# Kernel tuning notes

Hardware: AMD Instinct MI355X
Metric: run time of the kernel (lower is better)

Reference implementation:

```python
import jax, jax.numpy as jnp
import numpy as np

B, IN, OUT, G = 8192, 512, 512, 20


def setup_inputs() -> dict:
    key = jax.random.key(0)
    k1, k2, k3 = jax.random.split(key, 3)
    x = jax.random.normal(k1, (B, IN), dtype=jnp.float32)
    coeffs = jax.random.normal(k2, (OUT, IN, G + 1), dtype=jnp.float32) * 0.1
    base_w = jax.random.normal(k3, (OUT, IN), dtype=jnp.float32) * 0.1
    return {"x": x, "coeffs": coeffs, "base_w": base_w}


def reference(x, coeffs, base_w):
    g = coeffs.shape[-1] - 1  # grid_size
    xc = jnp.clip(x, -1.0, 1.0)
    base = jax.nn.silu(xc) @ base_w.T  # [B, out]
    x_grid = (xc + 1.0) * 0.5 * g  # [B, in], in [0, g]
    idx = jnp.clip(jnp.floor(x_grid).astype(jnp.int32), 0, g - 1)  # [B, in]
    t = x_grid - idx.astype(x.dtype)  # [B, in]
    b, n = x.shape
    bi = jnp.arange(b)[:, None]
    fi = jnp.arange(n)[None, :]
    # Sparse interpolation weights over grid bins: 2 nonzeros per (b, i).
    w = jnp.zeros((b, n, g + 1), dtype=x.dtype)
    w = w.at[bi, fi, idx].add(1.0 - t)
    w = w.at[bi, fi, idx + 1].add(t)  # idx+1 <= g since idx <= g-1
    # y[b,o] = sum_i sum_g w[b,i,g] * coeffs[o,i,g]
    y = jnp.einsum('big,oig->bo', w, coeffs)
    return base + y
```

## Files before the change

### kernel.cpp

```cpp
#include <hip/hip_runtime.h>
#include <stdint.h>


typedef short v8s __attribute__((ext_vector_type(8)));
typedef float v4f __attribute__((ext_vector_type(4)));

#define B_DIM 8192
#define IN_DIM 512
#define OUT_DIM 512
#define G_DIM 20
#define FPT 4
#define KT_TOTAL (IN_DIM / FPT)
#define KSPLIT 3
#define BM 128
#define BN 128
#define CHUNKS 12
#define PLANE 2048
#define TILE_BYTES (CHUNKS * PLANE)

#define P_BYTES ((size_t)IN_DIM * B_DIM * 8)
#define WT_BYTES ((size_t)(OUT_DIM / BN) * KT_TOTAL * TILE_BYTES)
#define PART_ELEMS ((size_t)B_DIM * OUT_DIM)
#define WS_NEED (P_BYTES + WT_BYTES + (size_t)KSPLIT * PART_ELEMS * 2)

#define PACK_BLKS ((B_DIM / 64) * (IN_DIM / 64))
#define WPACK_BLKS ((OUT_DIM * IN_DIM) / 256)

static __device__ __forceinline__ unsigned f2bf(float f) {
  unsigned u = __builtin_bit_cast(unsigned, f);
  return (u + 0x7fffu + ((u >> 16) & 1u)) >> 16;
}

static __device__ __forceinline__ float bflo(unsigned u) {
  return __builtin_bit_cast(float, u << 16);
}
static __device__ __forceinline__ float bfhi(unsigned u) {
  return __builtin_bit_cast(float, u & 0xffff0000u);
}

__global__ void zero_out_kernel(uint4* __restrict__ out) {
  out[(size_t)blockIdx.x * 256 + threadIdx.x] = uint4{0u, 0u, 0u, 0u};
}

__global__ void pack_fused_kernel(const float* __restrict__ x, uint2* __restrict__ P,
                                  const float* __restrict__ coeffs,
                                  const float* __restrict__ base_w,
                                  char* __restrict__ Wt) {
  __shared__ uint2 tile[64 * 65];
  const int t = threadIdx.x;
  if (blockIdx.x < PACK_BLKS) {
    const int b0 = (blockIdx.x & (B_DIM / 64 - 1)) * 64;
    const int i0 = (blockIdx.x / (B_DIM / 64)) * 64;
    const int tr = t >> 6;
    const int tc = t & 63;
#pragma unroll
    for (int it = 0; it < 16; ++it) {
      int br = it * 4 + tr;
      float xv = x[(size_t)(b0 + br) * IN_DIM + i0 + tc];
      float xc = fminf(fmaxf(xv, -1.0f), 1.0f);
      float xg = (xc + 1.0f) * 10.0f;
      int idx = (int)floorf(xg);
      idx = idx < 0 ? 0 : (idx > G_DIM - 1 ? G_DIM - 1 : idx);
      float tt = xg - (float)idx;
      float sl = xc / (1.0f + __expf(-xc));
      uint2 pv;
      pv.x = f2bf(1.0f - tt) | (f2bf(tt) << 16);
      pv.y = (unsigned)idx | (f2bf(sl) << 16);
      tile[tc * 65 + br] = pv;
    }
    __syncthreads();
#pragma unroll
    for (int it = 0; it < 16; ++it) {
      int ir = it * 4 + tr;
      P[(size_t)(i0 + ir) * B_DIM + b0 + tc] = tile[ir * 65 + tc];
    }
  } else {
    const unsigned u = (blockIdx.x - PACK_BLKS) * 256 + t;
    const int s = u >> 9;
    const int w = u & 511;
    const int row = w >> 2;
    const int f = w & 3;
    const int n_blk = s / KT_TOTAL;
    const int kt = s - n_blk * KT_TOTAL;
    const int o = n_blk * 128 + row;
    const int i = kt * 4 + f;
    const size_t g = (size_t)o * IN_DIM + i;
    const float* c = coeffs + g * 21;
    float cf[21];
#pragma unroll
    for (int j = 0; j < 21; ++j) cf[j] = c[j];
    float bw = base_w[g];
    unsigned d[12];
#pragma unroll
    for (int j = 0; j < 10; ++j) d[j] = f2bf(cf[2 * j]) | (f2bf(cf[2 * j + 1]) << 16);
    d[10] = f2bf(cf[20]) | (f2bf(bw) << 16);
    d[11] = 0u;
    char* slab = Wt + (size_t)s * TILE_BYTES;
#pragma unroll
    for (int p = 0; p < 3; ++p)
      *(uint4*)(slab + (3 * f + p) * PLANE + row * 16) =
          uint4{d[4 * p], d[4 * p + 1], d[4 * p + 2], d[4 * p + 3]};
  }
}

__global__ void reduce_kernel(const uint4* __restrict__ p, v4f* __restrict__ out) {
  size_t i = (size_t)blockIdx.x * 256 + threadIdx.x;
  const size_t q = PART_ELEMS / 8;
  uint4 a = p[i], b = p[i + q], c = p[i + 2 * q];
  v4f lo, hi;
  lo[0] = bflo(a.x) + bflo(b.x) + bflo(c.x);
  hi[0] = bfhi(a.x) + bfhi(b.x) + bfhi(c.x);
  lo[1] = bflo(a.y) + bflo(b.y) + bflo(c.y);
  hi[1] = bfhi(a.y) + bfhi(b.y) + bfhi(c.y);
  lo[2] = bflo(a.z) + bflo(b.z) + bflo(c.z);
  hi[2] = bfhi(a.z) + bfhi(b.z) + bfhi(c.z);
  lo[3] = bflo(a.w) + bflo(b.w) + bflo(c.w);
  hi[3] = bfhi(a.w) + bfhi(b.w) + bfhi(c.w);
  v4f o0 = {lo[0], hi[0], lo[1], hi[1]};
  v4f o1 = {lo[2], hi[2], lo[3], hi[3]};
  out[2 * i] = o0;
  out[2 * i + 1] = o1;
}

static __device__ __forceinline__ void stage_strip(char* abase, uint2 pv) {
  const uint4 zz = {0u, 0u, 0u, 0u};
#pragma unroll
  for (int p = 0; p < 3; ++p) *(uint4*)(abase + p * PLANE) = zz;
  const int idx = (int)(pv.y & 0xffffu);
  const int s1 = idx + 1;
  *(unsigned short*)(abase + ((idx >> 3) << 11) + ((idx & 7) << 1)) =
      (unsigned short)pv.x;
  *(unsigned short*)(abase + ((s1 >> 3) << 11) + ((s1 & 7) << 1)) =
      (unsigned short)(pv.x >> 16);
  *(unsigned short*)(abase + 2 * PLANE + 10) = (unsigned short)(pv.y >> 16);
}

template <bool ATOMIC>
__global__ __launch_bounds__(256, 3) void kan_gemm(const uint2* __restrict__ P,
                                                   const char* __restrict__ Wt,
                                                   unsigned short* __restrict__ part,
                                                   float* __restrict__ outA) {
  __shared__ uint4 lds4[TILE_BYTES / 16];
  char* Ab = (char*)lds4;
  const int t = threadIdx.x;
  const int lane = t & 63;
  const int wv = t >> 6;
  const int wm = wv >> 1, wn = wv & 1;
  const int b0 = blockIdx.x * BM;
  const int n_blk = blockIdx.y;
  const int z = blockIdx.z;
  const int kt0 = (z * KT_TOTAL) / KSPLIT;
  const int ktend = ((z + 1) * KT_TOTAL) / KSPLIT;

  v4f acc[4][4];
  const v4f z4 = {0.f, 0.f, 0.f, 0.f};
#pragma unroll
  for (int ii = 0; ii < 4; ++ii)
#pragma unroll
    for (int jj = 0; jj < 4; ++jj) acc[ii][jj] = z4;

  char* abase0 = Ab + 3 * wv * PLANE + lane * 16;
  char* abase1 = Ab + 3 * wv * PLANE + (lane + 64) * 16;
  uint2 pv0 = P[(size_t)(kt0 * 4 + wv) * B_DIM + b0 + lane];
  uint2 pv1 = P[(size_t)(kt0 * 4 + wv) * B_DIM + b0 + lane + 64];

  const int r16 = lane & 15;
  const int q16 = lane >> 4;

  const uint4* wbase = (const uint4*)(Wt + (size_t)n_blk * KT_TOTAL * TILE_BYTES);
  int bidx[3][4];
#pragma unroll
  for (int s = 0; s < 3; ++s)
#pragma unroll
    for (int cn = 0; cn < 4; ++cn)
      bidx[s][cn] = (s * 4 + q16) * 128 + wn * 64 + cn * 16 + r16;

  for (int kt = kt0; kt < ktend; ++kt) {
    __syncthreads();

    const uint4* wsrc = wbase + (size_t)kt * (TILE_BYTES / 16);
    uint4 bv[3][4];
#pragma unroll
    for (int s = 0; s < 3; ++s)
#pragma unroll
      for (int cn = 0; cn < 4; ++cn)
        bv[s][cn] = wsrc[bidx[s][cn]];

    const int ktn = (kt + 1 < ktend) ? kt + 1 : kt;
    uint2 pn0 = P[(size_t)(ktn * 4 + wv) * B_DIM + b0 + lane];
    uint2 pn1 = P[(size_t)(ktn * 4 + wv) * B_DIM + b0 + lane + 64];

    stage_strip(abase0, pv0);
    stage_strip(abase1, pv1);
    pv0 = pn0;
    pv1 = pn1;

    __syncthreads();

#pragma unroll
    for (int s = 0; s < 3; ++s) {
      const int chunk = s * 4 + q16;
      v8s af[4];
#pragma unroll
      for (int rm = 0; rm < 4; ++rm) {
        int row = wm * 64 + rm * 16 + r16;
        af[rm] = *(const v8s*)(Ab + chunk * PLANE + row * 16);
      }
#pragma unroll
      for (int rm = 0; rm < 4; ++rm)
#pragma unroll
        for (int cn = 0; cn < 4; ++cn)
          acc[rm][cn] = __builtin_amdgcn_mfma_f32_16x16x32_bf16(
              af[rm], __builtin_bit_cast(v8s, bv[s][cn]), acc[rm][cn], 0, 0, 0);
    }
  }

  const int q4 = (lane >> 4) * 4;
  if (ATOMIC) {
#pragma unroll
    for (int rm = 0; rm < 4; ++rm)
#pragma unroll
      for (int cn = 0; cn < 4; ++cn)
#pragma unroll
        for (int r = 0; r < 4; ++r) {
          int row = b0 + wm * 64 + rm * 16 + q4 + r;
          int col = n_blk * BN + wn * 64 + cn * 16 + r16;
          atomicAdd(outA + (size_t)row * OUT_DIM + col, acc[rm][cn][r]);
        }
  } else {
    unsigned short* mypart = part + (size_t)z * PART_ELEMS;
#pragma unroll
    for (int rm = 0; rm < 4; ++rm)
#pragma unroll
      for (int cn = 0; cn < 4; ++cn)
#pragma unroll
        for (int r = 0; r < 4; ++r) {
          int row = b0 + wm * 64 + rm * 16 + q4 + r;
          int col = n_blk * BN + wn * 64 + cn * 16 + r16;
          mypart[(size_t)row * OUT_DIM + col] = (unsigned short)f2bf(acc[rm][cn][r]);
        }
  }
}

extern "C" void kernel_launch(void* const* d_in, const int* in_sizes, int n_in,
                              void* d_out, int out_size, void* d_ws, size_t ws_size,
                              hipStream_t stream) {
  const float* x = (const float*)d_in[0];
  const float* coeffs = (const float*)d_in[1];
  const float* base_w = (const float*)d_in[2];
  float* out = (float*)d_out;

  uint2* P = (uint2*)d_ws;
  char* Wt = (char*)d_ws + P_BYTES;
  unsigned short* part = (unsigned short*)((char*)d_ws + P_BYTES + WT_BYTES);

  pack_fused_kernel<<<PACK_BLKS + WPACK_BLKS, 256, 0, stream>>>(x, P, coeffs, base_w, Wt);

  if (ws_size >= WS_NEED) {
    kan_gemm<false><<<dim3(B_DIM / BM, OUT_DIM / BN, KSPLIT), 256, 0, stream>>>(P, Wt, part, out);
    reduce_kernel<<<(int)(PART_ELEMS / 8 / 256), 256, 0, stream>>>((const uint4*)part, (v4f*)out);
  } else {
    zero_out_kernel<<<(int)((PART_ELEMS * 4) / 4096), 256, 0, stream>>>((uint4*)out);
    kan_gemm<true><<<dim3(B_DIM / BM, OUT_DIM / BN, KSPLIT), 256, 0, stream>>>(P, Wt, part, out);
  }
}
```

Measured before the change: 180.5 us.

## Double-buffer LDS A-tile and prefetch weights to remove per-iteration barrier

The shared A-tile becomes two buffers, so staging for step k+1 overlaps the MFMA work of step k. This leaves one __syncthreads per iteration instead of two. Weight fragments for the next k-step are loaded into registers after the current MFMAs, giving them a full iteration to arrive. Instead of zeroing three 16-byte planes per strip each step, each thread now clears only the two slots it wrote previously in that buffer. The cost is double the LDS use (48KB per block with 3 blocks per CU requested), plus extra live registers for the prefetched weights and cursor pointers.

```diff
diff --git a/kernel.cpp b/kernel.cpp
--- a/kernel.cpp
+++ b/kernel.cpp
@@ -122,17 +122,22 @@
   out[2 * i + 1] = o1;
 }
 
-static __device__ __forceinline__ void stage_strip(char* abase, uint2 pv) {
-  const uint4 zz = {0u, 0u, 0u, 0u};
-#pragma unroll
-  for (int p = 0; p < 3; ++p) *(uint4*)(abase + p * PLANE) = zz;
+static __device__ __forceinline__ int slot_off(int slot) {
+  return ((slot >> 3) << 11) + ((slot & 7) << 1);
+}
+
+static __device__ __forceinline__ void stage_inc(char* abase, uint2 pv,
+                                                 char*& ca, char*& cb) {
+  *(unsigned short*)ca = 0;
+  *(unsigned short*)cb = 0;
   const int idx = (int)(pv.y & 0xffffu);
-  const int s1 = idx + 1;
-  *(unsigned short*)(abase + ((idx >> 3) << 11) + ((idx & 7) << 1)) =
-      (unsigned short)pv.x;
-  *(unsigned short*)(abase + ((s1 >> 3) << 11) + ((s1 & 7) << 1)) =
-      (unsigned short)(pv.x >> 16);
+  char* wa = abase + slot_off(idx);
+  char* wb = abase + slot_off(idx + 1);
+  *(unsigned short*)wa = (unsigned short)pv.x;
+  *(unsigned short*)wb = (unsigned short)(pv.x >> 16);
   *(unsigned short*)(abase + 2 * PLANE + 10) = (unsigned short)(pv.y >> 16);
+  ca = wa;
+  cb = wb;
 }
 
 template <bool ATOMIC>
@@ -140,8 +145,7 @@
                                                    const char* __restrict__ Wt,
                                                    unsigned short* __restrict__ part,
                                                    float* __restrict__ outA) {
-  __shared__ uint4 lds4[TILE_BYTES / 16];
-  char* Ab = (char*)lds4;
+  __shared__ uint4 lds4[2 * TILE_BYTES / 16];
   const int t = threadIdx.x;
   const int lane = t & 63;
   const int wv = t >> 6;
@@ -159,10 +163,35 @@
 #pragma unroll
     for (int jj = 0; jj < 4; ++jj) acc[ii][jj] = z4;
 
-  char* abase0 = Ab + 3 * wv * PLANE + lane * 16;
-  char* abase1 = Ab + 3 * wv * PLANE + (lane + 64) * 16;
-  uint2 pv0 = P[(size_t)(kt0 * 4 + wv) * B_DIM + b0 + lane];
-  uint2 pv1 = P[(size_t)(kt0 * 4 + wv) * B_DIM + b0 + lane + 64];
+  {
+    const uint4 zz = {0u, 0u, 0u, 0u};
+#pragma unroll
+    for (int j = 0; j < 12; ++j) lds4[t + 256 * j] = zz;
+  }
+  __syncthreads();
+
+  char* ab0[2];
+  char* ab1[2];
+#pragma unroll
+  for (int p = 0; p < 2; ++p) {
+    ab0[p] = (char*)lds4 + p * TILE_BYTES + 3 * wv * PLANE + lane * 16;
+    ab1[p] = (char*)lds4 + p * TILE_BYTES + 3 * wv * PLANE + (lane + 64) * 16;
+  }
+  char* c0a[2] = {ab0[0], ab0[1]};
+  char* c0b[2] = {ab0[0] + 2, ab0[1] + 2};
+  char* c1a[2] = {ab1[0], ab1[1]};
+  char* c1b[2] = {ab1[0] + 2, ab1[1] + 2};
+
+  {
+    const int p0 = kt0 & 1;
+    uint2 s0 = P[(size_t)(kt0 * 4 + wv) * B_DIM + b0 + lane];
+    uint2 s1 = P[(size_t)(kt0 * 4 + wv) * B_DIM + b0 + lane + 64];
+    stage_inc(ab0[p0], s0, c0a[p0], c0b[p0]);
+    stage_inc(ab1[p0], s1, c1a[p0], c1b[p0]);
+  }
+  const int ktp = (kt0 + 1 < ktend) ? kt0 + 1 : ktend - 1;
+  uint2 pv0 = P[(size_t)(ktp * 4 + wv) * B_DIM + b0 + lane];
+  uint2 pv1 = P[(size_t)(ktp * 4 + wv) * B_DIM + b0 + lane + 64];
 
   const int r16 = lane & 15;
   const int q16 = lane >> 4;
@@ -175,27 +204,18 @@
     for (int cn = 0; cn < 4; ++cn)
       bidx[s][cn] = (s * 4 + q16) * 128 + wn * 64 + cn * 16 + r16;
 
+  uint4 bv[3][4];
+#pragma unroll
+  for (int s = 0; s < 3; ++s)
+#pragma unroll
+    for (int cn = 0; cn < 4; ++cn)
+      bv[s][cn] = wbase[(size_t)kt0 * (TILE_BYTES / 16) + bidx[s][cn]];
+
+  __syncthreads();
+
   for (int kt = kt0; kt < ktend; ++kt) {
-    __syncthreads();
-
-    const uint4* wsrc = wbase + (size_t)kt * (TILE_BYTES / 16);
-    uint4 bv[3][4];
-#pragma unroll
-    for (int s = 0; s < 3; ++s)
-#pragma unroll
-      for (int cn = 0; cn < 4; ++cn)
-        bv[s][cn] = wsrc[bidx[s][cn]];
-
-    const int ktn = (kt + 1 < ktend) ? kt + 1 : kt;
-    uint2 pn0 = P[(size_t)(ktn * 4 + wv) * B_DIM + b0 + lane];
-    uint2 pn1 = P[(size_t)(ktn * 4 + wv) * B_DIM + b0 + lane + 64];
-
-    stage_strip(abase0, pv0);
-    stage_strip(abase1, pv1);
-    pv0 = pn0;
-    pv1 = pn1;
-
-    __syncthreads();
+    const char* cur = (const char*)lds4 + (kt & 1) * TILE_BYTES;
+    const int pn = (kt + 1) & 1;
 
 #pragma unroll
     for (int s = 0; s < 3; ++s) {
@@ -204,7 +224,7 @@
 #pragma unroll
       for (int rm = 0; rm < 4; ++rm) {
         int row = wm * 64 + rm * 16 + r16;
-        af[rm] = *(const v8s*)(Ab + chunk * PLANE + row * 16);
+        af[rm] = *(const v8s*)(cur + chunk * PLANE + row * 16);
       }
 #pragma unroll
       for (int rm = 0; rm < 4; ++rm)
@@ -213,6 +233,22 @@
           acc[rm][cn] = __builtin_amdgcn_mfma_f32_16x16x32_bf16(
               af[rm], __builtin_bit_cast(v8s, bv[s][cn]), acc[rm][cn], 0, 0, 0);
     }
+
+    const int ktn = (kt + 1 < ktend) ? kt + 1 : ktend - 1;
+#pragma unroll
+    for (int s = 0; s < 3; ++s)
+#pragma unroll
+      for (int cn = 0; cn < 4; ++cn)
+        bv[s][cn] = wbase[(size_t)ktn * (TILE_BYTES / 16) + bidx[s][cn]];
+
+    stage_inc(ab0[pn], pv0, c0a[pn], c0b[pn]);
+    stage_inc(ab1[pn], pv1, c1a[pn], c1b[pn]);
+
+    const int ktn2 = (kt + 2 < ktend) ? kt + 2 : ktend - 1;
+    pv0 = P[(size_t)(ktn2 * 4 + wv) * B_DIM + b0 + lane];
+    pv1 = P[(size_t)(ktn2 * 4 + wv) * B_DIM + b0 + lane + 64];
+
+    __syncthreads();
   }
 
   const int q4 = (lane >> 4) * 4;
```

After: 185.8 us. 2.9% more time.
